# Performance work log

Measured on AMD Instinct MI355X. Metric: run time of the kernel, lower is better.

Reference implementation:

```python
import jax, jax.numpy as jnp
import numpy as np
from itertools import combinations

# ---- Clifford algebra Cl(3,0): 8 blades ordered by grade, 4 grades ----
METRIC = (1.0, 1.0, 1.0)
_N = 3
D = 2 ** _N          # 8 blades
G = _N + 1           # 4 grades, subspaces [1,3,3,1]
EPS = 1e-6
INV_SQRT2 = 0.7071067811865476

def _build_algebra():
    blades = []
    for g in range(G):
        blades += list(combinations(range(_N), g))
    bitmaps = [sum(1 << i for i in b) for b in blades]
    idx = {bm: i for i, bm in enumerate(bitmaps)}
    grades = np.array([len(b) for b in blades], dtype=np.int64)
    cayley = np.zeros((D, D, D), dtype=np.float32)
    for ia, a in enumerate(bitmaps):
        for ib, b in enumerate(bitmaps):
            s = 1.0
            aa = a >> 1
            while aa:  # canonical reordering sign
                if bin(aa & b).count('1') & 1:
                    s = -s
                aa >>= 1
            for i in range(_N):  # metric contraction of repeated basis vectors
                if (a >> i) & (b >> i) & 1:
                    s *= METRIC[i]
            cayley[ia, idx[a ^ b], ib] = s
    paths = np.zeros((G, G, G), dtype=np.float32)  # grade triples with nonzero structure constants
    for gi in range(G):
        for gj in range(G):
            for gk in range(G):
                sub = cayley[np.ix_(grades == gi, grades == gj, grades == gk)]
                paths[gi, gj, gk] = float(np.any(sub != 0.0))
    onehot = (grades[:, None] == np.arange(G)[None, :]).astype(np.float32)  # [D,G]
    return cayley, grades, paths, onehot

_CAYLEY_np, GRADE, _PATHS_np, _ONEHOT_np = _build_algebra()
CAYLEY = jnp.asarray(_CAYLEY_np)   # [D,D,D]: (x*y)_j = x_i C_{ijk} y_k
PATHS = jnp.asarray(_PATHS_np)     # [G,G,G] mask
GONEHOT = jnp.asarray(_ONEHOT_np)  # [D,G]


def mv_linear(x, w, b=None):
    # x: [B,in,D]; w: [out,in,G] -> one weight per grade, shared across blades of the grade
    y = jnp.einsum('bmi,nmi->bni', x, w[..., GRADE])
    if b is not None:
        y = y.at[..., 0].add(b)  # bias lives on the scalar blade only
    return y


def grade_q(x):
    # per-grade quadratic form (Euclidean metric => sum of squares per grade): [B,C,G]
    return jnp.einsum('bci,ig->bcg', x * x, GONEHOT)


def normalization(x, a):
    # NormalizationLayer: sigmoid-interpolated per-grade norm division
    norms = jnp.sqrt(jnp.abs(grade_q(x)))                 # [B,C,G]
    norms = jax.nn.sigmoid(a)[None] * (norms - 1.0) + 1.0
    return x / (norms[..., GRADE] + EPS)


def mv_silu(x, a, b):
    # MVSiLU with invariant='mag2': gate = sigmoid(a*[scalar, q_1, q_2, q_3] + b)
    q = grade_q(x)
    inv = jnp.concatenate([x[..., :1], q[..., 1:]], axis=-1)  # [B,C,G]
    gate = jax.nn.sigmoid(a[None] * inv + b[None])
    return gate[..., GRADE] * x


def _blade_weight(wg):
    # grade-triple weights [...,G,G,G] masked by valid product paths, expanded to blades, fused with Cayley table
    wg = wg * PATHS
    wb = wg[..., GRADE[:, None, None], GRADE[None, :, None], GRADE[None, None, :]]
    return wb * CAYLEY


def fcgp(x, w_right, norm_a, w_left, b_left, w_gp):
    # FullyConnectedSteerableGeometricProductLayer
    xr = normalization(mv_linear(x, w_right), norm_a)
    Wc = _blade_weight(w_gp)                      # [out,in,D,D,D]
    pair = jnp.einsum('bni,bnk->bnik', x, xr)     # [B,in,D,D]
    prod = jnp.einsum('bnik,mnijk->bmj', pair, Wc)
    return (mv_linear(x, w_left, b_left) + prod) * INV_SQRT2


def sgp(x, w_right, norm_a, w_left, b_left, w_gp):
    # SteerableGeometricProductLayer (per-channel geometric product)
    xr = normalization(mv_linear(x, w_right), norm_a)
    Wc = _blade_weight(w_gp)                      # [C,D,D,D]
    prod = jnp.einsum('bni,nijk,bnk->bnj', x, Wc, xr)
    return (mv_linear(x, w_left, b_left) + prod) * INV_SQRT2


def setup_inputs() -> dict:
    B, IN, H, OUT = 4096, 512, 32, 9
    key = jax.random.key(0)
    ks = jax.random.split(key, 16)
    def rn(k, shape, scale):
        return jax.random.normal(k, shape, dtype=jnp.float32) * scale
    return {
        'x': rn(ks[0], (B, IN, D), 1.0),
        'w_right1': rn(ks[1], (IN, IN, G), (1.0 / IN) ** 0.5),
        'norm_a1': jnp.zeros((IN, G), jnp.float32),
        'w_left1': rn(ks[2], (H, IN, G), (1.0 / IN) ** 0.5),
        'b_left1': rn(ks[3], (H,), 0.01),
        'gp_w1': rn(ks[4], (H, IN, G, G, G), (1.0 / IN) ** 0.5),
        'silu_a': jnp.ones((H, G), jnp.float32),
        'silu_b': jnp.zeros((H, G), jnp.float32),
        'w_right2': rn(ks[5], (H, H, G), (1.0 / H) ** 0.5),
        'norm_a2': jnp.zeros((H, G), jnp.float32),
        'w_left2': rn(ks[6], (H, H, G), (1.0 / H) ** 0.5),
        'b_left2': rn(ks[7], (H,), 0.01),
        'gp_w2': rn(ks[8], (H, G, G, G), 1.0),
        'w_right3': rn(ks[9], (H, H, G), (1.0 / H) ** 0.5),
        'norm_a3': jnp.zeros((H, G), jnp.float32),
        'w_left3': rn(ks[10], (OUT, H, G), (1.0 / H) ** 0.5),
        'b_left3': rn(ks[11], (OUT,), 0.01),
        'gp_w3': rn(ks[12], (OUT, H, G, G, G), (1.0 / H) ** 0.5),
    }


def reference(x, w_right1, norm_a1, w_left1, b_left1, gp_w1, silu_a, silu_b,
              w_right2, norm_a2, w_left2, b_left2, gp_w2,
              w_right3, norm_a3, w_left3, b_left3, gp_w3):
    h = fcgp(x, w_right1, norm_a1, w_left1, b_left1, gp_w1)
    h = mv_silu(h, silu_a, silu_b)
    h = sgp(h, w_right2, norm_a2, w_left2, b_left2, gp_w2)
    h = mv_silu(h, silu_a, silu_b)   # shared activation params, used twice as in torch
    return fcgp(h, w_right3, norm_a3, w_left3, b_left3, gp_w3)
```

## Files before the change

### kernel.cpp

```cpp
#include <hip/hip_runtime.h>
#include <hip/hip_bf16.h>
#include <math.h>

#define INV_SQRT2F 0.70710678118654752440f
#define AS1 __attribute__((address_space(1)))
#define AS3 __attribute__((address_space(3)))

typedef __attribute__((ext_vector_type(8))) short short8;
typedef __attribute__((ext_vector_type(4))) float floatx4;

struct Tables {
  int   kof[8][8];
  float cs[8][8];
  int   widx[8][8];
};
constexpr int t_bm(int i){ constexpr int t[8] = {0,1,2,4,3,5,6,7}; return t[i]; }
constexpr int t_idx(int b){ constexpr int t[8] = {0,1,2,4,3,5,6,7}; return t[b]; }
constexpr int t_gr(int i){ constexpr int t[8] = {0,1,1,1,2,2,2,3}; return t[i]; }
constexpr int t_pc(int x){ int c=0; while(x){ c += x&1; x >>= 1; } return c; }
constexpr float t_sign(int a, int b){
  float s = 1.f; int aa = a >> 1;
  while(aa){ if(t_pc(aa & b) & 1) s = -s; aa >>= 1; }
  return s;
}
constexpr int   c_kof(int j,int i){ return t_idx(t_bm(i)^t_bm(j)); }
constexpr float c_cs(int j,int i){ return t_sign(t_bm(i), t_bm(c_kof(j,i))); }
constexpr int   c_widx(int j,int i){ return t_gr(i)*16 + t_gr(j)*4 + t_gr(c_kof(j,i)); }
constexpr Tables mkTables(){
  Tables T{};
  for(int j=0;j<8;j++) for(int i=0;i<8;i++){
    T.kof[j][i]  = c_kof(j,i);
    T.cs[j][i]   = c_cs(j,i);
    T.widx[j][i] = c_widx(j,i);
  }
  return T;
}
__device__ const Tables d_TB = mkTables();

__device__ __forceinline__ float rcpf(float v){ return __builtin_amdgcn_rcpf(v); }
__device__ __forceinline__ float sigf(float z){ return rcpf(1.f + __expf(-z)); }
__device__ __forceinline__ int gradeOfIdx(int i){ return (i==0)?0:((i<4)?1:((i<7)?2:3)); }
__device__ __forceinline__ short f2bf(float v){
  __hip_bfloat16 h = __float2bfloat16(v);
  short s; __builtin_memcpy(&s, &h, 2); return s;
}
__device__ __forceinline__ float bf2f(short s){
  unsigned int w = ((unsigned int)(unsigned short)s) << 16;
  float f; __builtin_memcpy(&f, &w, 4); return f;
}
__device__ __forceinline__ void norm8v(float* v, float4 na){
  float s0 = sigf(na.x)*(fabsf(v[0])-1.f)+1.f+1e-6f;
  float s1 = sigf(na.y)*(sqrtf(v[1]*v[1]+v[2]*v[2]+v[3]*v[3])-1.f)+1.f+1e-6f;
  float s2 = sigf(na.z)*(sqrtf(v[4]*v[4]+v[5]*v[5]+v[6]*v[6])-1.f)+1.f+1e-6f;
  float s3 = sigf(na.w)*(fabsf(v[7])-1.f)+1.f+1e-6f;
  float r0 = rcpf(s0), r1 = rcpf(s1), r2 = rcpf(s2), r3 = rcpf(s3);
  v[0]*=r0; v[1]*=r1; v[2]*=r1; v[3]*=r1; v[4]*=r2; v[5]*=r2; v[6]*=r2; v[7]*=r3;
}

__global__ __launch_bounds__(256) void pack_x(const float* __restrict__ x,
                                              __hip_bfloat16* __restrict__ xP){
  size_t e = (size_t)blockIdx.x*256 + threadIdx.x;
  float4 u0 = *(const float4*)(x + e*8);
  float4 u1 = *(const float4*)(x + e*8 + 4);
  float u[8] = {u0.x,u0.y,u0.z,u0.w,u1.x,u1.y,u1.z,u1.w};
  #pragma unroll
  for(int i=0;i<8;i++) xP[(size_t)i*2097152 + e] = __float2bfloat16(u[i]);
}

__global__ __launch_bounds__(256) void pack_misc(const float* __restrict__ w,
                                                 const float* __restrict__ gpw,
                                                 const float* __restrict__ wl,
                                                 const float* __restrict__ w2r,
                                                 const float* __restrict__ w2l,
                                                 const float* __restrict__ w3r,
                                                 const float* __restrict__ gw3,
                                                 const float* __restrict__ w3l,
                                                 __hip_bfloat16* __restrict__ wP,
                                                 __hip_bfloat16* __restrict__ Bpack,
                                                 __hip_bfloat16* __restrict__ wlP,
                                                 __hip_bfloat16* __restrict__ w2rP,
                                                 __hip_bfloat16* __restrict__ w2lP,
                                                 __hip_bfloat16* __restrict__ w3rP,
                                                 __hip_bfloat16* __restrict__ Bp3){
  const int bx = blockIdx.x;
  if(bx < 1024){
    size_t e = (size_t)bx*256 + threadIdx.x;
    float4 u = *(const float4*)(w + e*4);
    float v[4] = {u.x,u.y,u.z,u.w};
    #pragma unroll
    for(int g=0; g<4; g++) wP[(size_t)g*262144 + e] = __float2bfloat16(v[g]);
  } else if(bx < 1536){
    int t = (bx-1024)*256 + threadIdx.x;
    int j = t >> 14; int n = (t >> 5) & 511; int m = t & 31;
    int sp = n >> 6, nc = (n >> 2) & 15, q = n & 3;
    const float* src = gpw + ((size_t)m*512 + n)*64;
    short8 o;
    #pragma unroll
    for(int jj=0; jj<8; jj++){
      if(jj == j){
        #pragma unroll
        for(int i=0;i<8;i++) o[i] = f2bf(c_cs(jj,i) * src[c_widx(jj,i)]);
      }
    }
    *(short8*)(Bpack + (size_t)(sp*16+nc)*8192 + j*1024 + q*256 + m*8) = o;
  } else if(bx < 2048){
    int t2 = (bx-1536)*256 + threadIdx.x;
    int j = t2 >> 14; int m = (t2 >> 9) & 31; int n = t2 & 511;
    int g = gradeOfIdx(j);
    wlP[t2] = __float2bfloat16(wl[((size_t)m*512 + n)*4 + g]);
  } else if(bx < 2144){
    int t = (bx-2048)*256 + threadIdx.x;
    int which = t >> 13; int r = t & 8191;
    int j = r >> 10; int n = (r >> 5) & 31; int m = r & 31;
    int g = gradeOfIdx(j);
    const float* src = (which==0) ? w2r : (which==1) ? w2l : w3r;
    __hip_bfloat16* dst = (which==0) ? w2rP : (which==1) ? w2lP : w3rP;
    dst[r] = __float2bfloat16(src[((size_t)n*32 + m)*4 + g]);
  } else {
    int t2 = (bx-2144)*256 + threadIdx.x;
    if(t2 >= 36864) return;
    int j = t2 / 4608; int rem = t2 - j*4608;
    int mo = rem / 288; int k = rem - mo*288;
    float v = 0.f;
    if(mo < 9){
      if(k < 256){
        int n = k >> 3, i = k & 7;
        v = d_TB.cs[j][i] * gw3[((size_t)mo*32 + n)*64 + d_TB.widx[j][i]];
      } else {
        int n = k - 256;
        v = w3l[((size_t)mo*32 + n)*4 + gradeOfIdx(j)];
      }
    }
    Bp3[t2] = __float2bfloat16(v);
  }
}

__global__ __launch_bounds__(256) void k1_mfma(const __hip_bfloat16* __restrict__ xP,
                                               const __hip_bfloat16* __restrict__ wP,
                                               __hip_bfloat16* __restrict__ linrP){
  __shared__ __align__(16) char lds[32768];
  char* As = lds;
  char* Bs = lds + 16384;
  const int tid = threadIdx.x;
  const int l   = tid & 63;
  const int w   = tid >> 6;
  const int i   = blockIdx.z;
  const int g   = gradeOfIdx(i);
  const size_t b0 = (size_t)blockIdx.x * 128;
  const size_t n0 = (size_t)blockIdx.y * 128;
  const __hip_bfloat16* Ag = xP + (size_t)i*2097152;
  const __hip_bfloat16* Bg = wP + (size_t)g*262144;

  const int wave_m = (w & 1) * 64;
  const int wave_n = (w >> 1) * 64;
  const int srow = l >> 3;
  const int scol = ((l & 7) ^ srow) * 8;

  floatx4 acc[4][4] = {};

  for(int kt = 0; kt < 512; kt += 64){
    #pragma unroll
    for(int it=0; it<4; it++){
      int c   = it*4 + w;
      int row = c*8 + srow;
      const __hip_bfloat16* sa = Ag + (b0 + row)*512 + kt + scol;
      const __hip_bfloat16* sb = Bg + (n0 + row)*512 + kt + scol;
      __builtin_amdgcn_global_load_lds((const AS1 void*)sa, (AS3 void*)(As + c*1024 + l*16), 16, 0, 0);
      __builtin_amdgcn_global_load_lds((const AS1 void*)sb, (AS3 void*)(Bs + c*1024 + l*16), 16, 0, 0);
    }
    __syncthreads();
    #pragma unroll
    for(int ks=0; ks<2; ks++){
      short8 af[4], bf[4];
      #pragma unroll
      for(int f=0; f<4; f++){
        int rA = wave_m + f*16 + (l & 15);
        int ca = (ks*64 + (l>>4)*16) ^ ((rA & 7) << 4);
        af[f] = *(const short8*)(As + rA*128 + ca);
        int rB = wave_n + f*16 + (l & 15);
        int cb = (ks*64 + (l>>4)*16) ^ ((rB & 7) << 4);
        bf[f] = *(const short8*)(Bs + rB*128 + cb);
      }
      #pragma unroll
      for(int mf=0; mf<4; mf++){
        #pragma unroll
        for(int nf=0; nf<4; nf++){
          acc[mf][nf] = __builtin_amdgcn_mfma_f32_16x16x32_bf16(af[mf], bf[nf], acc[mf][nf], 0, 0, 0);
        }
      }
    }
    __syncthreads();
  }
  __hip_bfloat16* outp = linrP + (size_t)i*2097152;
  #pragma unroll
  for(int mf=0; mf<4; mf++){
    #pragma unroll
    for(int nf=0; nf<4; nf++){
      #pragma unroll
      for(int r=0; r<4; r++){
        size_t m = wave_m + mf*16 + ((l>>4)<<2) + r;
        size_t n = wave_n + nf*16 + (l & 15);
        outp[(b0+m)*512 + n0+n] = __float2bfloat16(acc[mf][nf][r]);
      }
    }
  }
}

__global__ __launch_bounds__(256) void k_left(const __hip_bfloat16* __restrict__ xP,
                                              const __hip_bfloat16* __restrict__ wlP,
                                              float* __restrict__ leftB){
  const int tid = threadIdx.x;
  const int l = tid & 63, w = tid >> 6;
  const int j = blockIdx.y;
  const int row = blockIdx.x*64 + w*16 + (l & 15);
  floatx4 acc[2] = {};
  const __hip_bfloat16* Ap = xP + (size_t)j*2097152;
  const __hip_bfloat16* Wp = wlP + (size_t)j*16384;
  for(int nc=0; nc<16; nc++){
    int nb = nc*32 + (l>>4)*8;
    short8 a  = *(const short8*)(Ap + (size_t)row*512 + nb);
    short8 b0 = *(const short8*)(Wp + (l&15)*512 + nb);
    short8 b1 = *(const short8*)(Wp + ((l&15)+16)*512 + nb);
    acc[0] = __builtin_amdgcn_mfma_f32_16x16x32_bf16(a, b0, acc[0], 0, 0, 0);
    acc[1] = __builtin_amdgcn_mfma_f32_16x16x32_bf16(a, b1, acc[1], 0, 0, 0);
  }
  #pragma unroll
  for(int mf=0; mf<2; mf++){
    #pragma unroll
    for(int r=0; r<4; r++){
      int b = blockIdx.x*64 + w*16 + (l>>4)*4 + r;
      leftB[(size_t)j*131072 + b*32 + mf*16 + (l&15)] = acc[mf][r];
    }
  }
}

__global__ __launch_bounds__(256) void knorm(const __hip_bfloat16* __restrict__ linrP,
                                             const float* __restrict__ norm_a,
                                             __hip_bfloat16* __restrict__ xrI){
  const size_t base = ((size_t)blockIdx.x*256 + threadIdx.x) * 8;
  const short* lp = (const short*)linrP;
  short8 v[8];
  #pragma unroll
  for(int i=0;i<8;i++) v[i] = *(const short8*)(lp + (size_t)i*2097152 + base);
  short8 o[8];
  #pragma unroll
  for(int s=0;s<8;s++){
    float u[8];
    #pragma unroll
    for(int i=0;i<8;i++) u[i] = bf2f(v[i][s]);
    int n = (int)((base + s) & 511);
    float4 na = *(const float4*)(norm_a + n*4);
    norm8v(u, na);
    #pragma unroll
    for(int i=0;i<8;i++) o[s][i] = f2bf(u[i]);
  }
  short* op = (short*)xrI;
  #pragma unroll
  for(int s=0;s<8;s++) *(short8*)(op + (base+s)*8) = o[s];
}

__global__ __launch_bounds__(256) void k2_mfma(const float* __restrict__ x,
                                               const __hip_bfloat16* __restrict__ xrI,
                                               const __hip_bfloat16* __restrict__ Bpack,
                                               float* __restrict__ h1part){
  const int tid = threadIdx.x;
  const int l = tid & 63, w = tid >> 6;
  const int row = blockIdx.x*64 + w*16 + (l & 15);
  const int nsb = blockIdx.y * 64;
  const int boff = (l>>4)*256 + (l&15)*8;
  floatx4 acc[8][2] = {};

  for(int nc = 0; nc < 16; nc++){
    const int n = nsb + nc*4 + (l>>4);
    const size_t e = (size_t)row*512 + n;
    float4 xa = *(const float4*)(x + e*8);
    float4 xb = *(const float4*)(x + e*8 + 4);
    float xv[8] = {xa.x,xa.y,xa.z,xa.w,xb.x,xb.y,xb.z,xb.w};
    short8 xri = *(const short8*)((const short*)xrI + e*8);
    float xr[8];
    #pragma unroll
    for(int i=0;i<8;i++) xr[i] = bf2f(xri[i]);
    const __hip_bfloat16* bp_nc = Bpack + (size_t)(blockIdx.y*16 + nc)*8192 + boff;
    #pragma unroll
    for(int j=0;j<8;j++){
      short8 af;
      #pragma unroll
      for(int i=0;i<8;i++) af[i] = f2bf(xv[i] * xr[c_kof(j,i)]);
      short8 b0 = *(const short8*)(bp_nc + j*1024);
      short8 b1 = *(const short8*)(bp_nc + j*1024 + 128);
      acc[j][0] = __builtin_amdgcn_mfma_f32_16x16x32_bf16(af, b0, acc[j][0], 0, 0, 0);
      acc[j][1] = __builtin_amdgcn_mfma_f32_16x16x32_bf16(af, b1, acc[j][1], 0, 0, 0);
    }
  }
  const int sp = blockIdx.y;
  #pragma unroll
  for(int j=0;j<8;j++){
    #pragma unroll
    for(int mf=0; mf<2; mf++){
      #pragma unroll
      for(int r=0; r<4; r++){
        int b = blockIdx.x*64 + w*16 + (l>>4)*4 + r;
        h1part[((size_t)(sp*8+j))*131072 + b*32 + mf*16 + (l&15)] = acc[j][mf][r];
      }
    }
  }
}

__global__ __launch_bounds__(256) void k2b_silu(const float* __restrict__ h1part,
                                                const float* __restrict__ leftB,
                                                const float* __restrict__ bl,
                                                const float* __restrict__ sa,
                                                const float* __restrict__ sb,
                                                float* __restrict__ h1s,
                                                __hip_bfloat16* __restrict__ h1P){
  int idx = blockIdx.x*256 + threadIdx.x;
  int m = idx & 31;
  float v[8];
  #pragma unroll
  for(int j=0;j<8;j++){
    float s = leftB[(size_t)j*131072 + idx];
    #pragma unroll
    for(int sp=0; sp<8; sp++) s += h1part[((size_t)(sp*8+j))*131072 + idx];
    v[j] = s;
  }
  v[0] += bl[m];
  #pragma unroll
  for(int i=0;i<8;i++) v[i] *= INV_SQRT2F;
  float q1 = v[1]*v[1]+v[2]*v[2]+v[3]*v[3];
  float q2 = v[4]*v[4]+v[5]*v[5]+v[6]*v[6];
  float q3 = v[7]*v[7];
  float4 sa4 = *(const float4*)&sa[m*4];
  float4 sb4 = *(const float4*)&sb[m*4];
  float g0 = sigf(sa4.x*v[0] + sb4.x);
  float g1 = sigf(sa4.y*q1   + sb4.y);
  float g2 = sigf(sa4.z*q2   + sb4.z);
  float g3 = sigf(sa4.w*q3   + sb4.w);
  float o[8] = {g0*v[0], g1*v[1], g1*v[2], g1*v[3], g2*v[4], g2*v[5], g2*v[6], g3*v[7]};
  *(float4*)&h1s[(size_t)idx*8]     = make_float4(o[0],o[1],o[2],o[3]);
  *(float4*)&h1s[(size_t)idx*8 + 4] = make_float4(o[4],o[5],o[6],o[7]);
  #pragma unroll
  for(int j=0;j<8;j++) h1P[(size_t)j*131072 + idx] = __float2bfloat16(o[j]);
}

__global__ __launch_bounds__(256) void k3a(const __hip_bfloat16* __restrict__ h1P,
                                           const __hip_bfloat16* __restrict__ w2rP,
                                           const __hip_bfloat16* __restrict__ w2lP,
                                           float* __restrict__ linr2,
                                           float* __restrict__ left2){
  const int tid = threadIdx.x;
  const int l = tid & 63, w = tid >> 6;
  const int j = blockIdx.y;
  const int row = blockIdx.x*64 + w*16 + (l & 15);
  const int ko = (l>>4)*8;
  short8 a   = *(const short8*)(h1P + (size_t)j*131072 + (size_t)row*32 + ko);
  short8 br0 = *(const short8*)(w2rP + j*1024 + (l&15)*32 + ko);
  short8 br1 = *(const short8*)(w2rP + j*1024 + ((l&15)+16)*32 + ko);
  short8 bl0 = *(const short8*)(w2lP + j*1024 + (l&15)*32 + ko);
  short8 bl1 = *(const short8*)(w2lP + j*1024 + ((l&15)+16)*32 + ko);
  floatx4 aR0 = {}, aR1 = {}, aL0 = {}, aL1 = {};
  aR0 = __builtin_amdgcn_mfma_f32_16x16x32_bf16(a, br0, aR0, 0, 0, 0);
  aR1 = __builtin_amdgcn_mfma_f32_16x16x32_bf16(a, br1, aR1, 0, 0, 0);
  aL0 = __builtin_amdgcn_mfma_f32_16x16x32_bf16(a, bl0, aL0, 0, 0, 0);
  aL1 = __builtin_amdgcn_mfma_f32_16x16x32_bf16(a, bl1, aL1, 0, 0, 0);
  #pragma unroll
  for(int r=0; r<4; r++){
    int b = blockIdx.x*64 + w*16 + (l>>4)*4 + r;
    linr2[(size_t)j*131072 + b*32 + (l&15)]      = aR0[r];
    linr2[(size_t)j*131072 + b*32 + 16 + (l&15)] = aR1[r];
    left2[(size_t)j*131072 + b*32 + (l&15)]      = aL0[r];
    left2[(size_t)j*131072 + b*32 + 16 + (l&15)] = aL1[r];
  }
}

__global__ __launch_bounds__(256) void k3b(const float* __restrict__ linr2,
                                           const float* __restrict__ left2,
                                           const float* __restrict__ h1s,
                                           const float* __restrict__ na2,
                                           const float* __restrict__ gw2,
                                           const float* __restrict__ b2l,
                                           const float* __restrict__ sa,
                                           const float* __restrict__ sb,
                                           float* __restrict__ h2f,
                                           __hip_bfloat16* __restrict__ h2P){
  int idx = blockIdx.x*256 + threadIdx.x;
  int n = idx & 31;
  float x2[8];
  #pragma unroll
  for(int j=0;j<8;j++) x2[j] = linr2[(size_t)j*131072 + idx];
  norm8v(x2, *(const float4*)&na2[n*4]);
  float4 h0 = *(const float4*)&h1s[(size_t)idx*8];
  float4 h1 = *(const float4*)&h1s[(size_t)idx*8 + 4];
  float h[8] = {h0.x,h0.y,h0.z,h0.w,h1.x,h1.y,h1.z,h1.w};
  const float* g2 = gw2 + (size_t)n*64;
  float v[8];
  #pragma unroll
  for(int j=0;j<8;j++){
    float pr = 0.f;
    #pragma unroll
    for(int i=0;i<8;i++)
      pr = fmaf(c_cs(j,i) * h[i] * x2[c_kof(j,i)], g2[c_widx(j,i)], pr);
    v[j] = (pr + left2[(size_t)j*131072 + idx] + ((j==0) ? b2l[n] : 0.f)) * INV_SQRT2F;
  }
  float q1 = v[1]*v[1]+v[2]*v[2]+v[3]*v[3];
  float q2 = v[4]*v[4]+v[5]*v[5]+v[6]*v[6];
  float q3 = v[7]*v[7];
  float4 sa4 = *(const float4*)&sa[n*4];
  float4 sb4 = *(const float4*)&sb[n*4];
  float g0 = sigf(sa4.x*v[0] + sb4.x);
  float g1 = sigf(sa4.y*q1   + sb4.y);
  float gg2 = sigf(sa4.z*q2  + sb4.z);
  float g3 = sigf(sa4.w*q3   + sb4.w);
  float o[8] = {g0*v[0], g1*v[1], g1*v[2], g1*v[3], gg2*v[4], gg2*v[5], gg2*v[6], g3*v[7]};
  *(float4*)&h2f[(size_t)idx*8]     = make_float4(o[0],o[1],o[2],o[3]);
  *(float4*)&h2f[(size_t)idx*8 + 4] = make_float4(o[4],o[5],o[6],o[7]);
  #pragma unroll
  for(int j=0;j<8;j++) h2P[(size_t)j*131072 + idx] = __float2bfloat16(o[j]);
}

__global__ __launch_bounds__(256) void k3c(const __hip_bfloat16* __restrict__ h2P,
                                           const __hip_bfloat16* __restrict__ w3rP,
                                           float* __restrict__ linr3){
  const int tid = threadIdx.x;
  const int l = tid & 63, w = tid >> 6;
  const int j = blockIdx.y;
  const int row = blockIdx.x*64 + w*16 + (l & 15);
  const int ko = (l>>4)*8;
  short8 a   = *(const short8*)(h2P + (size_t)j*131072 + (size_t)row*32 + ko);
  short8 b0  = *(const short8*)(w3rP + j*1024 + (l&15)*32 + ko);
  short8 b1  = *(const short8*)(w3rP + j*1024 + ((l&15)+16)*32 + ko);
  floatx4 a0 = {}, a1 = {};
  a0 = __builtin_amdgcn_mfma_f32_16x16x32_bf16(a, b0, a0, 0, 0, 0);
  a1 = __builtin_amdgcn_mfma_f32_16x16x32_bf16(a, b1, a1, 0, 0, 0);
  #pragma unroll
  for(int r=0; r<4; r++){
    int b = blockIdx.x*64 + w*16 + (l>>4)*4 + r;
    linr3[(size_t)j*131072 + b*32 + (l&15)]      = a0[r];
    linr3[(size_t)j*131072 + b*32 + 16 + (l&15)] = a1[r];
  }
}

__global__ __launch_bounds__(256) void k3d(const float* __restrict__ linr3,
                                           const float* __restrict__ h2f,
                                           const float* __restrict__ na3,
                                           __hip_bfloat16* __restrict__ pairP){
  int idx = blockIdx.x*256 + threadIdx.x;
  int n = idx & 31;
  float x3[8];
  #pragma unroll
  for(int j=0;j<8;j++) x3[j] = linr3[(size_t)j*131072 + idx];
  norm8v(x3, *(const float4*)&na3[n*4]);
  float4 h0 = *(const float4*)&h2f[(size_t)idx*8];
  float4 h1 = *(const float4*)&h2f[(size_t)idx*8 + 4];
  float h[8] = {h0.x,h0.y,h0.z,h0.w,h1.x,h1.y,h1.z,h1.w};
  #pragma unroll
  for(int j=0;j<8;j++){
    short8 o;
    #pragma unroll
    for(int i=0;i<8;i++) o[i] = f2bf(h[i] * x3[c_kof(j,i)]);
    *(short8*)(pairP + (size_t)j*1048576 + (size_t)idx*8) = o;
  }
}

__global__ __launch_bounds__(256) void k3e(const __hip_bfloat16* __restrict__ pairP,
                                           const __hip_bfloat16* __restrict__ h2P,
                                           const __hip_bfloat16* __restrict__ Bp3,
                                           const float* __restrict__ b3l,
                                           float* __restrict__ out){
  const int tid = threadIdx.x;
  const int l = tid & 63, w = tid >> 6;
  const int j = blockIdx.y;
  const int row = blockIdx.x*64 + w*16 + (l & 15);
  const int mo = l & 15;
  const int ko = (l>>4)*8;
  floatx4 acc = {};
  const __hip_bfloat16* Ap = pairP + (size_t)j*1048576 + (size_t)row*256;
  const __hip_bfloat16* Bp = Bp3 + (size_t)j*4608 + mo*288;
  #pragma unroll
  for(int kc=0; kc<8; kc++){
    short8 a = *(const short8*)(Ap + kc*32 + ko);
    short8 b = *(const short8*)(Bp + kc*32 + ko);
    acc = __builtin_amdgcn_mfma_f32_16x16x32_bf16(a, b, acc, 0, 0, 0);
  }
  {
    short8 a = *(const short8*)(h2P + (size_t)j*131072 + (size_t)row*32 + ko);
    short8 b = *(const short8*)(Bp + 256 + ko);
    acc = __builtin_amdgcn_mfma_f32_16x16x32_bf16(a, b, acc, 0, 0, 0);
  }
  if(mo < 9){
    #pragma unroll
    for(int r=0; r<4; r++){
      int b = blockIdx.x*64 + w*16 + (l>>4)*4 + r;
      out[((size_t)b*9 + mo)*8 + j] = (acc[r] + ((j==0) ? b3l[mo] : 0.f)) * INV_SQRT2F;
    }
  }
}

extern "C" void kernel_launch(void* const* d_in, const int* in_sizes, int n_in,
                              void* d_out, int out_size, void* d_ws, size_t ws_size,
                              hipStream_t stream){
  const float* x        = (const float*)d_in[0];
  const float* w_right1 = (const float*)d_in[1];
  const float* norm_a1  = (const float*)d_in[2];
  const float* w_left1  = (const float*)d_in[3];
  const float* b_left1  = (const float*)d_in[4];
  const float* gp_w1    = (const float*)d_in[5];
  const float* silu_a   = (const float*)d_in[6];
  const float* silu_b   = (const float*)d_in[7];
  const float* w_right2 = (const float*)d_in[8];
  const float* norm_a2  = (const float*)d_in[9];
  const float* w_left2  = (const float*)d_in[10];
  const float* b_left2  = (const float*)d_in[11];
  const float* gp_w2    = (const float*)d_in[12];
  const float* w_right3 = (const float*)d_in[13];
  const float* norm_a3  = (const float*)d_in[14];
  const float* w_left3  = (const float*)d_in[15];
  const float* b_left3  = (const float*)d_in[16];
  const float* gp_w3    = (const float*)d_in[17];
  float* out = (float*)d_out;

  char* wsb = (char*)d_ws;
  __hip_bfloat16* xP    = (__hip_bfloat16*)wsb;
  __hip_bfloat16* xrI   = (__hip_bfloat16*)wsb;
  __hip_bfloat16* pairP = (__hip_bfloat16*)wsb;
  float*          linr2 = (float*)(wsb + 16777216);
  float*          left2 = (float*)(wsb + 20971520);
  float*          h2f   = (float*)(wsb + 25165824);
  __hip_bfloat16* h2P   = (__hip_bfloat16*)(wsb + 29360128);
  __hip_bfloat16* wP    = (__hip_bfloat16*)(wsb + 33554432);
  __hip_bfloat16* h1P   = (__hip_bfloat16*)(wsb + 33554432);
  float*          h1s   = (float*)(wsb + 35651584);
  __hip_bfloat16* linrP = (__hip_bfloat16*)(wsb + 41943040);
  float*          h1part= (float*)(wsb + 41943040);
  float*          linr3 = (float*)(wsb + 41943040);
  __hip_bfloat16* Bpack = (__hip_bfloat16*)(wsb + 75497472);
  __hip_bfloat16* wlP   = (__hip_bfloat16*)(wsb + 77594624);
  float*          leftB = (float*)(wsb + 77856768);
  __hip_bfloat16* w2rP  = (__hip_bfloat16*)(wsb + 82051072);
  __hip_bfloat16* w2lP  = (__hip_bfloat16*)(wsb + 82051072 + 16384);
  __hip_bfloat16* w3rP  = (__hip_bfloat16*)(wsb + 82051072 + 32768);
  __hip_bfloat16* Bp3   = (__hip_bfloat16*)(wsb + 82051072 + 49152);

  pack_x<<<8192, 256, 0, stream>>>(x, xP);
  pack_misc<<<2288, 256, 0, stream>>>(w_right1, gp_w1, w_left1,
                                      w_right2, w_left2, w_right3, gp_w3, w_left3,
                                      wP, Bpack, wlP, w2rP, w2lP, w3rP, Bp3);
  k1_mfma<<<dim3(32, 4, 8), 256, 0, stream>>>(xP, wP, linrP);
  k_left<<<dim3(64, 8), 256, 0, stream>>>(xP, wlP, leftB);
  knorm<<<1024, 256, 0, stream>>>(linrP, norm_a1, xrI);
  k2_mfma<<<dim3(64, 8), 256, 0, stream>>>(x, xrI, Bpack, h1part);
  k2b_silu<<<512, 256, 0, stream>>>(h1part, leftB, b_left1, silu_a, silu_b, h1s, h1P);
  k3a<<<dim3(64, 8), 256, 0, stream>>>(h1P, w2rP, w2lP, linr2, left2);
  k3b<<<512, 256, 0, stream>>>(linr2, left2, h1s, norm_a2, gp_w2, b_left2,
                               silu_a, silu_b, h2f, h2P);
  k3c<<<dim3(64, 8), 256, 0, stream>>>(h2P, w3rP, linr3);
  k3d<<<512, 256, 0, stream>>>(linr3, h2f, norm_a3, pairP);
  k3e<<<dim3(64, 8), 256, 0, stream>>>(pairP, h2P, Bp3, b_left3, out);
}
```

Measured before the change: 153.9 us.

## Fuse second-layer MFMA GEMMs with their elementwise normalization and product epilogues

Merges k3a with k3b, and k3c with k3d, so each block computes all 8 blade GEMMs into registers and applies the normalization, geometric-product, SiLU or pair-formation epilogue directly on the accumulators. This removes the float intermediates linr2, left2 and linr3, saving their global write and read traffic and two kernel launches. The cost is a grid reduced to 64 blocks, each thread doing eight times more epilogue work with many live accumulators, which risks poor occupancy and GPU under-utilisation. The Bpack index expression is also simplified to an equivalent form.

```diff
diff --git a/kernel.cpp b/kernel.cpp
--- a/kernel.cpp
+++ b/kernel.cpp
@@ -92,7 +92,6 @@
   } else if(bx < 1536){
     int t = (bx-1024)*256 + threadIdx.x;
     int j = t >> 14; int n = (t >> 5) & 511; int m = t & 31;
-    int sp = n >> 6, nc = (n >> 2) & 15, q = n & 3;
     const float* src = gpw + ((size_t)m*512 + n)*64;
     short8 o;
     #pragma unroll
@@ -102,7 +101,8 @@
         for(int i=0;i<8;i++) o[i] = f2bf(c_cs(jj,i) * src[c_widx(jj,i)]);
       }
     }
-    *(short8*)(Bpack + (size_t)(sp*16+nc)*8192 + j*1024 + q*256 + m*8) = o;
+    int q = n & 3;
+    *(short8*)(Bpack + (size_t)(n>>2)*8192 + j*1024 + q*256 + m*8) = o;
   } else if(bx < 2048){
     int t2 = (bx-1536)*256 + threadIdx.x;
     int j = t2 >> 14; int m = (t2 >> 9) & 31; int n = t2 & 511;
@@ -342,122 +342,118 @@
   for(int j=0;j<8;j++) h1P[(size_t)j*131072 + idx] = __float2bfloat16(o[j]);
 }
 
-__global__ __launch_bounds__(256) void k3a(const __hip_bfloat16* __restrict__ h1P,
-                                           const __hip_bfloat16* __restrict__ w2rP,
-                                           const __hip_bfloat16* __restrict__ w2lP,
-                                           float* __restrict__ linr2,
-                                           float* __restrict__ left2){
+__global__ __launch_bounds__(256) void k3ab(const __hip_bfloat16* __restrict__ h1P,
+                                            const __hip_bfloat16* __restrict__ w2rP,
+                                            const __hip_bfloat16* __restrict__ w2lP,
+                                            const float* __restrict__ h1s,
+                                            const float* __restrict__ na2,
+                                            const float* __restrict__ gw2,
+                                            const float* __restrict__ b2l,
+                                            const float* __restrict__ sa,
+                                            const float* __restrict__ sb,
+                                            float* __restrict__ h2f,
+                                            __hip_bfloat16* __restrict__ h2P){
   const int tid = threadIdx.x;
   const int l = tid & 63, w = tid >> 6;
-  const int j = blockIdx.y;
   const int row = blockIdx.x*64 + w*16 + (l & 15);
   const int ko = (l>>4)*8;
-  short8 a   = *(const short8*)(h1P + (size_t)j*131072 + (size_t)row*32 + ko);
-  short8 br0 = *(const short8*)(w2rP + j*1024 + (l&15)*32 + ko);
-  short8 br1 = *(const short8*)(w2rP + j*1024 + ((l&15)+16)*32 + ko);
-  short8 bl0 = *(const short8*)(w2lP + j*1024 + (l&15)*32 + ko);
-  short8 bl1 = *(const short8*)(w2lP + j*1024 + ((l&15)+16)*32 + ko);
-  floatx4 aR0 = {}, aR1 = {}, aL0 = {}, aL1 = {};
-  aR0 = __builtin_amdgcn_mfma_f32_16x16x32_bf16(a, br0, aR0, 0, 0, 0);
-  aR1 = __builtin_amdgcn_mfma_f32_16x16x32_bf16(a, br1, aR1, 0, 0, 0);
-  aL0 = __builtin_amdgcn_mfma_f32_16x16x32_bf16(a, bl0, aL0, 0, 0, 0);
-  aL1 = __builtin_amdgcn_mfma_f32_16x16x32_bf16(a, bl1, aL1, 0, 0, 0);
-  #pragma unroll
-  for(int r=0; r<4; r++){
-    int b = blockIdx.x*64 + w*16 + (l>>4)*4 + r;
-    linr2[(size_t)j*131072 + b*32 + (l&15)]      = aR0[r];
-    linr2[(size_t)j*131072 + b*32 + 16 + (l&15)] = aR1[r];
-    left2[(size_t)j*131072 + b*32 + (l&15)]      = aL0[r];
-    left2[(size_t)j*131072 + b*32 + 16 + (l&15)] = aL1[r];
-  }
-}
-
-__global__ __launch_bounds__(256) void k3b(const float* __restrict__ linr2,
-                                           const float* __restrict__ left2,
-                                           const float* __restrict__ h1s,
-                                           const float* __restrict__ na2,
-                                           const float* __restrict__ gw2,
-                                           const float* __restrict__ b2l,
-                                           const float* __restrict__ sa,
-                                           const float* __restrict__ sb,
-                                           float* __restrict__ h2f,
-                                           __hip_bfloat16* __restrict__ h2P){
-  int idx = blockIdx.x*256 + threadIdx.x;
-  int n = idx & 31;
-  float x2[8];
-  #pragma unroll
-  for(int j=0;j<8;j++) x2[j] = linr2[(size_t)j*131072 + idx];
-  norm8v(x2, *(const float4*)&na2[n*4]);
-  float4 h0 = *(const float4*)&h1s[(size_t)idx*8];
-  float4 h1 = *(const float4*)&h1s[(size_t)idx*8 + 4];
-  float h[8] = {h0.x,h0.y,h0.z,h0.w,h1.x,h1.y,h1.z,h1.w};
-  const float* g2 = gw2 + (size_t)n*64;
-  float v[8];
+  floatx4 xacc[8][2], lacc[8][2];
   #pragma unroll
   for(int j=0;j<8;j++){
-    float pr = 0.f;
-    #pragma unroll
-    for(int i=0;i<8;i++)
-      pr = fmaf(c_cs(j,i) * h[i] * x2[c_kof(j,i)], g2[c_widx(j,i)], pr);
-    v[j] = (pr + left2[(size_t)j*131072 + idx] + ((j==0) ? b2l[n] : 0.f)) * INV_SQRT2F;
-  }
-  float q1 = v[1]*v[1]+v[2]*v[2]+v[3]*v[3];
-  float q2 = v[4]*v[4]+v[5]*v[5]+v[6]*v[6];
-  float q3 = v[7]*v[7];
-  float4 sa4 = *(const float4*)&sa[n*4];
-  float4 sb4 = *(const float4*)&sb[n*4];
-  float g0 = sigf(sa4.x*v[0] + sb4.x);
-  float g1 = sigf(sa4.y*q1   + sb4.y);
-  float gg2 = sigf(sa4.z*q2  + sb4.z);
-  float g3 = sigf(sa4.w*q3   + sb4.w);
-  float o[8] = {g0*v[0], g1*v[1], g1*v[2], g1*v[3], gg2*v[4], gg2*v[5], gg2*v[6], g3*v[7]};
-  *(float4*)&h2f[(size_t)idx*8]     = make_float4(o[0],o[1],o[2],o[3]);
-  *(float4*)&h2f[(size_t)idx*8 + 4] = make_float4(o[4],o[5],o[6],o[7]);
-  #pragma unroll
-  for(int j=0;j<8;j++) h2P[(size_t)j*131072 + idx] = __float2bfloat16(o[j]);
-}
-
-__global__ __launch_bounds__(256) void k3c(const __hip_bfloat16* __restrict__ h2P,
-                                           const __hip_bfloat16* __restrict__ w3rP,
-                                           float* __restrict__ linr3){
+    short8 a   = *(const short8*)(h1P + (size_t)j*131072 + (size_t)row*32 + ko);
+    short8 br0 = *(const short8*)(w2rP + j*1024 + (l&15)*32 + ko);
+    short8 br1 = *(const short8*)(w2rP + j*1024 + ((l&15)+16)*32 + ko);
+    short8 bl0 = *(const short8*)(w2lP + j*1024 + (l&15)*32 + ko);
+    short8 bl1 = *(const short8*)(w2lP + j*1024 + ((l&15)+16)*32 + ko);
+    floatx4 z0 = {}, z1 = {}, z2 = {}, z3 = {};
+    xacc[j][0] = __builtin_amdgcn_mfma_f32_16x16x32_bf16(a, br0, z0, 0, 0, 0);
+    xacc[j][1] = __builtin_amdgcn_mfma_f32_16x16x32_bf16(a, br1, z1, 0, 0, 0);
+    lacc[j][0] = __builtin_amdgcn_mfma_f32_16x16x32_bf16(a, bl0, z2, 0, 0, 0);
+    lacc[j][1] = __builtin_amdgcn_mfma_f32_16x16x32_bf16(a, bl1, z3, 0, 0, 0);
+  }
+  #pragma unroll
+  for(int h=0; h<2; h++){
+    #pragma unroll
+    for(int r=0; r<4; r++){
+      int b = blockIdx.x*64 + w*16 + (l>>4)*4 + r;
+      int n = h*16 + (l & 15);
+      size_t idx = (size_t)b*32 + n;
+      float x2[8], lf[8];
+      #pragma unroll
+      for(int j=0;j<8;j++){ x2[j] = xacc[j][h][r]; lf[j] = lacc[j][h][r]; }
+      norm8v(x2, *(const float4*)&na2[n*4]);
+      float4 h0 = *(const float4*)&h1s[idx*8];
+      float4 h1v = *(const float4*)&h1s[idx*8 + 4];
+      float hh[8] = {h0.x,h0.y,h0.z,h0.w,h1v.x,h1v.y,h1v.z,h1v.w};
+      const float* g2 = gw2 + (size_t)n*64;
+      float v[8];
+      #pragma unroll
+      for(int j=0;j<8;j++){
+        float pr = 0.f;
+        #pragma unroll
+        for(int i=0;i<8;i++)
+          pr = fmaf(c_cs(j,i) * hh[i] * x2[c_kof(j,i)], g2[c_widx(j,i)], pr);
+        v[j] = (pr + lf[j] + ((j==0) ? b2l[n] : 0.f)) * INV_SQRT2F;
+      }
+      float q1 = v[1]*v[1]+v[2]*v[2]+v[3]*v[3];
+      float q2 = v[4]*v[4]+v[5]*v[5]+v[6]*v[6];
+      float q3 = v[7]*v[7];
+      float4 sa4 = *(const float4*)&sa[n*4];
+      float4 sb4 = *(const float4*)&sb[n*4];
+      float g0 = sigf(sa4.x*v[0] + sb4.x);
+      float g1 = sigf(sa4.y*q1   + sb4.y);
+      float gg2 = sigf(sa4.z*q2  + sb4.z);
+      float g3 = sigf(sa4.w*q3   + sb4.w);
+      float o[8] = {g0*v[0], g1*v[1], g1*v[2], g1*v[3], gg2*v[4], gg2*v[5], gg2*v[6], g3*v[7]};
+      *(float4*)&h2f[idx*8]     = make_float4(o[0],o[1],o[2],o[3]);
+      *(float4*)&h2f[idx*8 + 4] = make_float4(o[4],o[5],o[6],o[7]);
+      #pragma unroll
+      for(int j=0;j<8;j++) h2P[(size_t)j*131072 + idx] = __float2bfloat16(o[j]);
+    }
+  }
+}
+
+__global__ __launch_bounds__(256) void k3cd(const __hip_bfloat16* __restrict__ h2P,
+                                            const __hip_bfloat16* __restrict__ w3rP,
+                                            const float* __restrict__ h2f,
+                                            const float* __restrict__ na3,
+                                            __hip_bfloat16* __restrict__ pairP){
   const int tid = threadIdx.x;
   const int l = tid & 63, w = tid >> 6;
-  const int j = blockIdx.y;
   const int row = blockIdx.x*64 + w*16 + (l & 15);
   const int ko = (l>>4)*8;
-  short8 a   = *(const short8*)(h2P + (size_t)j*131072 + (size_t)row*32 + ko);
-  short8 b0  = *(const short8*)(w3rP + j*1024 + (l&15)*32 + ko);
-  short8 b1  = *(const short8*)(w3rP + j*1024 + ((l&15)+16)*32 + ko);
-  floatx4 a0 = {}, a1 = {};
-  a0 = __builtin_amdgcn_mfma_f32_16x16x32_bf16(a, b0, a0, 0, 0, 0);
-  a1 = __builtin_amdgcn_mfma_f32_16x16x32_bf16(a, b1, a1, 0, 0, 0);
-  #pragma unroll
-  for(int r=0; r<4; r++){
-    int b = blockIdx.x*64 + w*16 + (l>>4)*4 + r;
-    linr3[(size_t)j*131072 + b*32 + (l&15)]      = a0[r];
-    linr3[(size_t)j*131072 + b*32 + 16 + (l&15)] = a1[r];
-  }
-}
-
-__global__ __launch_bounds__(256) void k3d(const float* __restrict__ linr3,
-                                           const float* __restrict__ h2f,
-                                           const float* __restrict__ na3,
-                                           __hip_bfloat16* __restrict__ pairP){
-  int idx = blockIdx.x*256 + threadIdx.x;
-  int n = idx & 31;
-  float x3[8];
-  #pragma unroll
-  for(int j=0;j<8;j++) x3[j] = linr3[(size_t)j*131072 + idx];
-  norm8v(x3, *(const float4*)&na3[n*4]);
-  float4 h0 = *(const float4*)&h2f[(size_t)idx*8];
-  float4 h1 = *(const float4*)&h2f[(size_t)idx*8 + 4];
-  float h[8] = {h0.x,h0.y,h0.z,h0.w,h1.x,h1.y,h1.z,h1.w};
+  floatx4 xacc[8][2];
   #pragma unroll
   for(int j=0;j<8;j++){
-    short8 o;
-    #pragma unroll
-    for(int i=0;i<8;i++) o[i] = f2bf(h[i] * x3[c_kof(j,i)]);
-    *(short8*)(pairP + (size_t)j*1048576 + (size_t)idx*8) = o;
+    short8 a  = *(const short8*)(h2P + (size_t)j*131072 + (size_t)row*32 + ko);
+    short8 b0 = *(const short8*)(w3rP + j*1024 + (l&15)*32 + ko);
+    short8 b1 = *(const short8*)(w3rP + j*1024 + ((l&15)+16)*32 + ko);
+    floatx4 z0 = {}, z1 = {};
+    xacc[j][0] = __builtin_amdgcn_mfma_f32_16x16x32_bf16(a, b0, z0, 0, 0, 0);
+    xacc[j][1] = __builtin_amdgcn_mfma_f32_16x16x32_bf16(a, b1, z1, 0, 0, 0);
+  }
+  #pragma unroll
+  for(int h=0; h<2; h++){
+    #pragma unroll
+    for(int r=0; r<4; r++){
+      int b = blockIdx.x*64 + w*16 + (l>>4)*4 + r;
+      int n = h*16 + (l & 15);
+      size_t idx = (size_t)b*32 + n;
+      float x3[8];
+      #pragma unroll
+      for(int j=0;j<8;j++) x3[j] = xacc[j][h][r];
+      norm8v(x3, *(const float4*)&na3[n*4]);
+      float4 h0 = *(const float4*)&h2f[idx*8];
+      float4 h1v = *(const float4*)&h2f[idx*8 + 4];
+      float hh[8] = {h0.x,h0.y,h0.z,h0.w,h1v.x,h1v.y,h1v.z,h1v.w};
+      #pragma unroll
+      for(int j=0;j<8;j++){
+        short8 o;
+        #pragma unroll
+        for(int i=0;i<8;i++) o[i] = f2bf(hh[i] * x3[c_kof(j,i)]);
+        *(short8*)(pairP + (size_t)j*1048576 + idx*8) = o;
+      }
+    }
   }
 }
 
@@ -522,8 +518,6 @@
   __hip_bfloat16* xP    = (__hip_bfloat16*)wsb;
   __hip_bfloat16* xrI   = (__hip_bfloat16*)wsb;
   __hip_bfloat16* pairP = (__hip_bfloat16*)wsb;
-  float*          linr2 = (float*)(wsb + 16777216);
-  float*          left2 = (float*)(wsb + 20971520);
   float*          h2f   = (float*)(wsb + 25165824);
   __hip_bfloat16* h2P   = (__hip_bfloat16*)(wsb + 29360128);
   __hip_bfloat16* wP    = (__hip_bfloat16*)(wsb + 33554432);
@@ -531,7 +525,6 @@
   float*          h1s   = (float*)(wsb + 35651584);
   __hip_bfloat16* linrP = (__hip_bfloat16*)(wsb + 41943040);
   float*          h1part= (float*)(wsb + 41943040);
-  float*          linr3 = (float*)(wsb + 41943040);
   __hip_bfloat16* Bpack = (__hip_bfloat16*)(wsb + 75497472);
   __hip_bfloat16* wlP   = (__hip_bfloat16*)(wsb + 77594624);
   float*          leftB = (float*)(wsb + 77856768);
@@ -549,10 +542,8 @@
   knorm<<<1024, 256, 0, stream>>>(linrP, norm_a1, xrI);
   k2_mfma<<<dim3(64, 8), 256, 0, stream>>>(x, xrI, Bpack, h1part);
   k2b_silu<<<512, 256, 0, stream>>>(h1part, leftB, b_left1, silu_a, silu_b, h1s, h1P);
-  k3a<<<dim3(64, 8), 256, 0, stream>>>(h1P, w2rP, w2lP, linr2, left2);
-  k3b<<<512, 256, 0, stream>>>(linr2, left2, h1s, norm_a2, gp_w2, b_left2,
+  k3ab<<<64, 256, 0, stream>>>(h1P, w2rP, w2lP, h1s, norm_a2, gp_w2, b_left2,
                                silu_a, silu_b, h2f, h2P);
-  k3c<<<dim3(64, 8), 256, 0, stream>>>(h2P, w3rP, linr3);
-  k3d<<<512, 256, 0, stream>>>(linr3, h2f, norm_a3, pairP);
+  k3cd<<<64, 256, 0, stream>>>(h2P, w3rP, h2f, norm_a3, pairP);
   k3e<<<dim3(64, 8), 256, 0, stream>>>(pairP, h2P, Bp3, b_left3, out);
 }
```

Result: slower. 169.0 us (+9.8%).
